# Optimization experiments

Measured on AMD Instinct MI355X. Metric: run time of the kernel, lower is better.

The kernel has to match this reference:

```python
import jax, jax.numpy as jnp
import numpy as np

N_EMBD = 1024
N_HEAD = 16
BLOCK_SIZE = 2048


def setup_inputs() -> dict:
    key = jax.random.key(0)
    k1, k2, k3 = jax.random.split(key, 3)
    B, T, C = 2, 2048, N_EMBD
    x = jax.random.normal(k1, (B, T, C), dtype=jnp.float32)
    # Dense(3*n_embd, use_bias=False): kernel [C, 3C]
    Wqkv = jax.random.normal(k2, (C, 3 * C), dtype=jnp.float32) * (1.0 / np.sqrt(C))
    # Output Dense(n_embd): kernel [C, C] + bias [C]
    Wout = jax.random.normal(k3, (C, C), dtype=jnp.float32) * (1.0 / np.sqrt(C))
    bout = jnp.zeros((C,), dtype=jnp.float32)
    return {"x": x, "Wqkv": Wqkv, "Wout": Wout, "bout": bout}


def reference(x, Wqkv, Wout, bout):
    B, T, C = x.shape
    H = N_HEAD
    hs = C // H  # head_size

    qkv = x @ Wqkv                       # [B, T, 3C]
    q, k, v = jnp.split(qkv, 3, axis=-1)  # each [B, T, C]
    q = q.reshape(B, T, H, hs).transpose(0, 2, 1, 3)  # [B, H, T, hs]
    k = k.reshape(B, T, H, hs).transpose(0, 2, 1, 3)
    v = v.reshape(B, T, H, hs).transpose(0, 2, 1, 3)

    att = jnp.einsum("bhqd,bhkd->bhqk", q, k) * (hs ** -0.5)  # [B, H, T, T]
    T_use = min(T, BLOCK_SIZE)
    mask = jnp.tril(jnp.ones((T_use, T_use), dtype=bool))
    att = jnp.where(mask, att, -jnp.inf)
    att = jax.nn.softmax(att, axis=-1)
    # dropout: deterministic (training=False) -> identity

    out = jnp.einsum("bhqk,bhkd->bhqd", att, v)  # [B, H, T, hs]
    out = out.transpose(0, 2, 1, 3).reshape(B, T, C)
    out = out @ Wout + bout
    return out
```

## Files before the change

### kernel.cpp

```cpp
#include <hip/hip_runtime.h>
#include <cstdint>
#include <cstddef>

#define BB 2
#define TT 2048
#define CC 1024
#define HH 16
#define HS 64
#define MM (BB*TT)
#define N1 (3*CC)

#define PST2 40

#define QSCALE 0.1803368801111243f

typedef __bf16 bf16_t;
typedef bf16_t bf16x8 __attribute__((ext_vector_type(8)));
typedef float  floatx4 __attribute__((ext_vector_type(4)));

__device__ __forceinline__ bf16_t f2bf(float f) {
    uint32_t u = __builtin_bit_cast(uint32_t, f);
    u += 0x7FFFu + ((u >> 16) & 1u);
    unsigned short s = (unsigned short)(u >> 16);
    return __builtin_bit_cast(bf16_t, s);
}

__device__ __forceinline__ void load_lds16(const bf16_t* g, bf16_t* l) {
    __builtin_amdgcn_global_load_lds((__attribute__((address_space(1))) void*)g,
                                     (__attribute__((address_space(3))) void*)l,
                                     16, 0, 0);
}

__global__ __launch_bounds__(256) void k_pack(const float* __restrict__ src,
                                              bf16_t* __restrict__ dst) {
    size_t i = ((size_t)blockIdx.x * 256 + threadIdx.x) * 8;
    float4 a = *(const float4*)(src + i);
    float4 b = *(const float4*)(src + i + 4);
    bf16x8 o;
    o[0] = f2bf(a.x); o[1] = f2bf(a.y); o[2] = f2bf(a.z); o[3] = f2bf(a.w);
    o[4] = f2bf(b.x); o[5] = f2bf(b.y); o[6] = f2bf(b.z); o[7] = f2bf(b.w);
    *(bf16x8*)(dst + i) = o;
}

__global__ __launch_bounds__(256) void k_transpose(const float* __restrict__ src,
                                                   bf16_t* __restrict__ dst,
                                                   int R, int Ccol) {
    __shared__ bf16_t tile[32][33];
    int c0 = blockIdx.x * 32, r0 = blockIdx.y * 32;
    int tx = threadIdx.x, ty = threadIdx.y;
    for (int i = ty; i < 32; i += 8)
        tile[i][tx] = f2bf(src[(size_t)(r0 + i) * Ccol + c0 + tx]);
    __syncthreads();
    for (int i = ty; i < 32; i += 8)
        dst[(size_t)(c0 + i) * R + r0 + tx] = tile[tx][i];
}

__device__ __forceinline__ void gemm_core(const bf16_t* __restrict__ A,
                                          const bf16_t* __restrict__ Bt,
                                          bf16_t* As, bf16_t* Bs,
                                          int m0, int n0, int K,
                                          floatx4 acc[4][4]) {
    const int tid = threadIdx.x;
    const int wave = tid >> 6, lane = tid & 63;
    const int quad = lane >> 4, lrow = lane & 15;
    const int wm = wave >> 1, wn = wave & 1;
    const int lsub = lane >> 2;
    const int kc = lane & 3;

    for (int kk = 0; kk < K; kk += 32) {
        for (int s = 0; s < 2; ++s) {
            int rg = wave * 2 + s;
            const bf16_t* ga = A  + (size_t)(m0 + rg * 16 + lsub) * K + kk + kc * 8;
            const bf16_t* gb = Bt + (size_t)(n0 + rg * 16 + lsub) * K + kk + kc * 8;
            load_lds16(ga, As + rg * 512);
            load_lds16(gb, Bs + rg * 512);
        }
        __syncthreads();
        bf16x8 af[4], bfr[4];
        for (int i = 0; i < 4; ++i)
            af[i] = *(const bf16x8*)(As + (wm * 64 + i * 16 + lrow) * 32 + quad * 8);
        for (int j = 0; j < 4; ++j)
            bfr[j] = *(const bf16x8*)(Bs + (wn * 64 + j * 16 + lrow) * 32 + quad * 8);
        for (int i = 0; i < 4; ++i)
            for (int j = 0; j < 4; ++j)
                acc[i][j] = __builtin_amdgcn_mfma_f32_16x16x32_bf16(af[i], bfr[j], acc[i][j], 0, 0, 0);
        __syncthreads();
    }
}

__global__ __launch_bounds__(256, 2) void k_gemm_qkv(const bf16_t* __restrict__ x,
                                                     const bf16_t* __restrict__ Wt,
                                                     bf16_t* __restrict__ qb,
                                                     bf16_t* __restrict__ kb,
                                                     bf16_t* __restrict__ vn) {
    __shared__ bf16_t As[128 * 32];
    __shared__ bf16_t Bs[128 * 32];
    const int m0 = blockIdx.y * 128, n0 = blockIdx.x * 128;
    floatx4 acc[4][4];
    for (int i = 0; i < 4; ++i)
        for (int j = 0; j < 4; ++j)
            acc[i][j] = floatx4{0.f, 0.f, 0.f, 0.f};
    gemm_core(x, Wt, As, Bs, m0, n0, CC, acc);

    const int tid = threadIdx.x, wave = tid >> 6, lane = tid & 63;
    const int quad = lane >> 4, lrow = lane & 15;
    const int wm = wave >> 1, wn = wave & 1;
    for (int i = 0; i < 4; ++i)
        for (int j = 0; j < 4; ++j) {
            int gn = n0 + wn * 64 + j * 16 + lrow;
            int which = gn >> 10, c = gn & 1023, h = c >> 6, d = c & 63;
            for (int r = 0; r < 4; ++r) {
                int gm = m0 + wm * 64 + i * 16 + quad * 4 + r;
                int b = gm >> 11, t = gm & 2047;
                float val = acc[i][j][r];
                if (which == 0)
                    qb[((size_t)(b * HH + h) * TT + t) * HS + d] = f2bf(val * QSCALE);
                else if (which == 1)
                    kb[((size_t)(b * HH + h) * TT + t) * HS + d] = f2bf(val);
                else
                    vn[((size_t)(b * HH + h) * TT + t) * HS + d] = f2bf(val);
            }
        }
}

__global__ __launch_bounds__(256) void k_vperm(const bf16_t* __restrict__ vn,
                                               bf16_t* __restrict__ vt) {
    __shared__ bf16_t tile[64][72];
    const int tid = threadIdx.x;
    const int bh = blockIdx.x & 31, tb = blockIdx.x >> 5;
    const bf16_t* src = vn + ((size_t)bh * TT + tb * 64) * HS;

    for (int h = 0; h < 2; ++h) {
        int r = (tid >> 3) + h * 32;
        int c8 = (tid & 7) * 8;
        *(bf16x8*)(&tile[r][c8]) = *(const bf16x8*)(src + (size_t)r * HS + c8);
    }
    __syncthreads();

    bf16_t* dst = vt + (size_t)bh * HS * TT + tb * 64;
    const int a   = tid & 15;
    const int blk = ((tid >> 4) & 1) * 32;
    const int dg  = tid >> 5;
    for (int k = 0; k < 8; ++k) {
        int d = dg * 8 + k;
        uint32_t lo = (uint32_t)__builtin_bit_cast(unsigned short, tile[blk + a][d]);
        uint32_t hi = (uint32_t)__builtin_bit_cast(unsigned short, tile[blk + a + 16][d]);
        *(uint32_t*)(dst + (size_t)d * TT + blk + 2 * a) = lo | (hi << 16);
    }
}

__global__ __launch_bounds__(128, 2) void k_attn(const bf16_t* __restrict__ qb,
                                                 const bf16_t* __restrict__ kb,
                                                 const bf16_t* __restrict__ vt,
                                                 bf16_t* __restrict__ y) {
    __shared__ bf16_t Kb[2][32 * 72];
    __shared__ bf16_t Vb[2][64 * 40];
    __shared__ bf16_t Ps[2][32 * PST2];
    const int tid = threadIdx.x;
    const int w = tid >> 6, lane = tid & 63;
    const int quad = lane >> 4, lrow = lane & 15;
    const int bh = blockIdx.x & 31;
    const int g = blockIdx.x >> 5;
    const int t2 = g >> 3, u = g & 7;
    const int qg = (t2 == 0) ? (31 - u) : (t2 == 1) ? u : (t2 == 2) ? (23 - u) : (8 + u);
    const int q0 = qg * 64 + w * 32;
    const int kend = qg * 2 + w + 1;
    const int ntmax = qg * 2 + 2;

    const bf16_t* Qg = qb + (size_t)bh * TT * HS;
    const bf16_t* Kg = kb + (size_t)bh * TT * HS;
    const bf16_t* Vg = vt + (size_t)bh * HS * TT;

    const int skey = tid >> 2, scol = (tid & 3) * 16;
    const int svrow = tid >> 1, svcol = (tid & 1) * 16;

    bf16x8 kra, krb, vra, vrb;
    {
        const bf16_t* gk = Kg + (size_t)skey * HS + scol;
        kra = *(const bf16x8*)(gk);
        krb = *(const bf16x8*)(gk + 8);
        const bf16_t* gv = Vg + (size_t)svrow * TT + svcol;
        vra = *(const bf16x8*)(gv);
        vrb = *(const bf16x8*)(gv + 8);
        *(bf16x8*)(&Kb[0][skey * 72 + scol])     = kra;
        *(bf16x8*)(&Kb[0][skey * 72 + scol + 8]) = krb;
        *(bf16x8*)(&Vb[0][svrow * 40 + svcol])     = vra;
        *(bf16x8*)(&Vb[0][svrow * 40 + svcol + 8]) = vrb;
    }

    bf16x8 aq[2][2];
    for (int tq = 0; tq < 2; ++tq)
        for (int c = 0; c < 2; ++c)
            aq[tq][c] = *(const bf16x8*)(Qg + (size_t)(q0 + tq * 16 + lrow) * HS + c * 32 + quad * 8);

    floatx4 o[2][4];
    for (int tq = 0; tq < 2; ++tq)
        for (int dc = 0; dc < 4; ++dc) o[tq][dc] = floatx4{0.f, 0.f, 0.f, 0.f};
    float lsum[2][4] = {{0.f,0.f,0.f,0.f},{0.f,0.f,0.f,0.f}};

    uint32_t* P32 = (uint32_t*)(&Ps[w][0]);
    const bf16_t* Pr = &Ps[w][0];
    const int wrow0 = quad * 4;

    for (int t = 0; t < ntmax; ++t) {
        __syncthreads();
        if (t + 1 < ntmax) {
            const bf16_t* gk = Kg + (size_t)((t + 1) * 32 + skey) * HS + scol;
            kra = *(const bf16x8*)(gk);
            krb = *(const bf16x8*)(gk + 8);
            const bf16_t* gv = Vg + (size_t)svrow * TT + (t + 1) * 32 + svcol;
            vra = *(const bf16x8*)(gv);
            vrb = *(const bf16x8*)(gv + 8);
        }
        if (t < kend) {
            const bf16_t* Kt = &Kb[t & 1][0];
            const bf16_t* Vt = &Vb[t & 1][0];
            bf16x8 bk0 = *(const bf16x8*)(Kt + lrow * 72 + quad * 8);
            bf16x8 bk1 = *(const bf16x8*)(Kt + lrow * 72 + 32 + quad * 8);
            bf16x8 bk2 = *(const bf16x8*)(Kt + (16 + lrow) * 72 + quad * 8);
            bf16x8 bk3 = *(const bf16x8*)(Kt + (16 + lrow) * 72 + 32 + quad * 8);
            floatx4 s00 = floatx4{0.f,0.f,0.f,0.f}, s01 = s00, s10 = s00, s11 = s00;
            s00 = __builtin_amdgcn_mfma_f32_16x16x32_bf16(aq[0][0], bk0, s00, 0, 0, 0);
            s00 = __builtin_amdgcn_mfma_f32_16x16x32_bf16(aq[0][1], bk1, s00, 0, 0, 0);
            s01 = __builtin_amdgcn_mfma_f32_16x16x32_bf16(aq[0][0], bk2, s01, 0, 0, 0);
            s01 = __builtin_amdgcn_mfma_f32_16x16x32_bf16(aq[0][1], bk3, s01, 0, 0, 0);
            s10 = __builtin_amdgcn_mfma_f32_16x16x32_bf16(aq[1][0], bk0, s10, 0, 0, 0);
            s10 = __builtin_amdgcn_mfma_f32_16x16x32_bf16(aq[1][1], bk1, s10, 0, 0, 0);
            s11 = __builtin_amdgcn_mfma_f32_16x16x32_bf16(aq[1][0], bk2, s11, 0, 0, 0);
            s11 = __builtin_amdgcn_mfma_f32_16x16x32_bf16(aq[1][1], bk3, s11, 0, 0, 0);

            bf16x8 bv0 = *(const bf16x8*)(Vt + (0  + lrow) * 40 + quad * 8);
            bf16x8 bv1 = *(const bf16x8*)(Vt + (16 + lrow) * 40 + quad * 8);
            bf16x8 bv2 = *(const bf16x8*)(Vt + (32 + lrow) * 40 + quad * 8);
            bf16x8 bv3 = *(const bf16x8*)(Vt + (48 + lrow) * 40 + quad * 8);

            if (t < kend - 1) {
                for (int r = 0; r < 4; ++r) {
                    float e00 = __builtin_amdgcn_exp2f(s00[r]);
                    float e01 = __builtin_amdgcn_exp2f(s01[r]);
                    float e10 = __builtin_amdgcn_exp2f(s10[r]);
                    float e11 = __builtin_amdgcn_exp2f(s11[r]);
                    lsum[0][r] += e00 + e01;
                    lsum[1][r] += e10 + e11;
                    uint32_t pk0 = __builtin_amdgcn_perm(
                        __builtin_bit_cast(uint32_t, e01) + 0x8000u,
                        __builtin_bit_cast(uint32_t, e00) + 0x8000u, 0x07060302u);
                    uint32_t pk1 = __builtin_amdgcn_perm(
                        __builtin_bit_cast(uint32_t, e11) + 0x8000u,
                        __builtin_bit_cast(uint32_t, e10) + 0x8000u, 0x07060302u);
                    P32[(wrow0 + r) * 20 + lrow]      = pk0;
                    P32[(wrow0 + r + 16) * 20 + lrow] = pk1;
                }
            } else {
                for (int r = 0; r < 4; ++r) {
                    bool keep = lrow <= quad * 4 + r;
                    float e00 = keep ? __builtin_amdgcn_exp2f(s00[r]) : 0.f;
                    float e01 = 0.f; (void)s01;
                    float e10 = __builtin_amdgcn_exp2f(s10[r]);
                    float e11 = keep ? __builtin_amdgcn_exp2f(s11[r]) : 0.f;
                    lsum[0][r] += e00 + e01;
                    lsum[1][r] += e10 + e11;
                    uint32_t pk0 = __builtin_amdgcn_perm(
                        __builtin_bit_cast(uint32_t, e01) + 0x8000u,
                        __builtin_bit_cast(uint32_t, e00) + 0x8000u, 0x07060302u);
                    uint32_t pk1 = __builtin_amdgcn_perm(
                        __builtin_bit_cast(uint32_t, e11) + 0x8000u,
                        __builtin_bit_cast(uint32_t, e10) + 0x8000u, 0x07060302u);
                    P32[(wrow0 + r) * 20 + lrow]      = pk0;
                    P32[(wrow0 + r + 16) * 20 + lrow] = pk1;
                }
            }
            asm volatile("s_waitcnt lgkmcnt(0)" ::: "memory");

            bf16x8 pa0 = *(const bf16x8*)(Pr + (size_t)lrow * PST2 + quad * 8);
            bf16x8 pa1 = *(const bf16x8*)(Pr + (size_t)(16 + lrow) * PST2 + quad * 8);
            o[0][0] = __builtin_amdgcn_mfma_f32_16x16x32_bf16(pa0, bv0, o[0][0], 0, 0, 0);
            o[0][1] = __builtin_amdgcn_mfma_f32_16x16x32_bf16(pa0, bv1, o[0][1], 0, 0, 0);
            o[0][2] = __builtin_amdgcn_mfma_f32_16x16x32_bf16(pa0, bv2, o[0][2], 0, 0, 0);
            o[0][3] = __builtin_amdgcn_mfma_f32_16x16x32_bf16(pa0, bv3, o[0][3], 0, 0, 0);
            o[1][0] = __builtin_amdgcn_mfma_f32_16x16x32_bf16(pa1, bv0, o[1][0], 0, 0, 0);
            o[1][1] = __builtin_amdgcn_mfma_f32_16x16x32_bf16(pa1, bv1, o[1][1], 0, 0, 0);
            o[1][2] = __builtin_amdgcn_mfma_f32_16x16x32_bf16(pa1, bv2, o[1][2], 0, 0, 0);
            o[1][3] = __builtin_amdgcn_mfma_f32_16x16x32_bf16(pa1, bv3, o[1][3], 0, 0, 0);
        }
        if (t + 1 < ntmax) {
            bf16_t* Kn = &Kb[(t + 1) & 1][0];
            bf16_t* Vn = &Vb[(t + 1) & 1][0];
            *(bf16x8*)(Kn + skey * 72 + scol)     = kra;
            *(bf16x8*)(Kn + skey * 72 + scol + 8) = krb;
            *(bf16x8*)(Vn + svrow * 40 + svcol)     = vra;
            *(bf16x8*)(Vn + svrow * 40 + svcol + 8) = vrb;
        }
    }

    const int b = bh >> 4, h = bh & 15;
    for (int tq = 0; tq < 2; ++tq)
        for (int r = 0; r < 4; ++r) {
            float s = lsum[tq][r];
            s += __shfl_xor(s, 1, 64);
            s += __shfl_xor(s, 2, 64);
            s += __shfl_xor(s, 4, 64);
            s += __shfl_xor(s, 8, 64);
            float inv = 1.0f / s;
            int q = q0 + tq * 16 + quad * 4 + r;
            for (int dc = 0; dc < 4; ++dc)
                y[(size_t)(b * TT + q) * CC + h * HS + dc * 16 + lrow] = f2bf(o[tq][dc][r] * inv);
        }
}

__global__ __launch_bounds__(256, 2) void k_gemm_out(const bf16_t* __restrict__ yin,
                                                     const bf16_t* __restrict__ Wt,
                                                     const float* __restrict__ bias,
                                                     float* __restrict__ out) {
    __shared__ bf16_t As[128 * 32];
    __shared__ bf16_t Bs[128 * 32];
    const int m0 = blockIdx.y * 128, n0 = blockIdx.x * 128;
    floatx4 acc[4][4];
    for (int i = 0; i < 4; ++i)
        for (int j = 0; j < 4; ++j)
            acc[i][j] = floatx4{0.f, 0.f, 0.f, 0.f};
    gemm_core(yin, Wt, As, Bs, m0, n0, CC, acc);

    const int tid = threadIdx.x, wave = tid >> 6, lane = tid & 63;
    const int quad = lane >> 4, lrow = lane & 15;
    const int wm = wave >> 1, wn = wave & 1;
    for (int i = 0; i < 4; ++i)
        for (int j = 0; j < 4; ++j) {
            int gn = n0 + wn * 64 + j * 16 + lrow;
            float bb = bias[gn];
            for (int r = 0; r < 4; ++r) {
                int gm = m0 + wm * 64 + i * 16 + quad * 4 + r;
                out[(size_t)gm * CC + gn] = acc[i][j][r] + bb;
            }
        }
}

extern "C" void kernel_launch(void* const* d_in, const int* in_sizes, int n_in,
                              void* d_out, int out_size, void* d_ws, size_t ws_size,
                              hipStream_t stream) {
    (void)in_sizes; (void)n_in; (void)out_size; (void)ws_size;
    const float* x    = (const float*)d_in[0];
    const float* Wqkv = (const float*)d_in[1];
    const float* Wout = (const float*)d_in[2];
    const float* bout = (const float*)d_in[3];
    float* out = (float*)d_out;

    bf16_t* xb  = (bf16_t*)d_ws;
    bf16_t* Wt1 = xb + (size_t)MM * CC;
    bf16_t* Wt2 = Wt1 + (size_t)N1 * CC;
    bf16_t* qb  = Wt2 + (size_t)CC * CC;
    bf16_t* kb  = qb + (size_t)BB * HH * TT * HS;
    bf16_t* vb  = kb + (size_t)BB * HH * TT * HS;
    bf16_t* yb  = vb + (size_t)BB * HH * TT * HS;
    bf16_t* vn  = yb;

    k_pack<<<dim3((size_t)MM * CC / (256 * 8)), 256, 0, stream>>>(x, xb);
    k_transpose<<<dim3(N1 / 32, CC / 32), dim3(32, 8), 0, stream>>>(Wqkv, Wt1, CC, N1);
    k_transpose<<<dim3(CC / 32, CC / 32), dim3(32, 8), 0, stream>>>(Wout, Wt2, CC, CC);
    k_gemm_qkv<<<dim3(N1 / 128, MM / 128), 256, 0, stream>>>(xb, Wt1, qb, kb, vn);
    k_vperm<<<dim3(32 * 32), 256, 0, stream>>>(vn, vb);
    k_attn<<<dim3(32 * 32), 128, 0, stream>>>(qb, kb, vb, yb);
    k_gemm_out<<<dim3(CC / 128, MM / 128), 256, 0, stream>>>(yb, Wt2, bout, out);
}
```

Measured before the change: 190.2 us.

## Split attention over key chunks with atomic accumulation and separate normalize pass

The attention kernel is now split along the key dimension into chunks of 256 keys, giving 144 blocks per head instead of 32. Partial unnormalized outputs and row sums are accumulated in fp32 with atomicAdd into scratch buffers, and a new k_norm kernel divides and packs the result to bf16. Row sums are computed by an extra MFMA against a vector of ones, and the bf16 rounding bias is dropped so P is truncated. The aim is better load balance and occupancy across the causal triangle, at the cost of two memsets, many atomics, an extra kernel and reuse of the output and weight buffers as scratch.

```diff
diff --git a/kernel.cpp b/kernel.cpp
--- a/kernel.cpp
+++ b/kernel.cpp
@@ -152,7 +152,8 @@
 __global__ __launch_bounds__(128, 2) void k_attn(const bf16_t* __restrict__ qb,
                                                  const bf16_t* __restrict__ kb,
                                                  const bf16_t* __restrict__ vt,
-                                                 bf16_t* __restrict__ y) {
+                                                 float* __restrict__ o_accum,
+                                                 float* __restrict__ l_acc) {
     __shared__ bf16_t Kb[2][32 * 72];
     __shared__ bf16_t Vb[2][64 * 40];
     __shared__ bf16_t Ps[2][32 * PST2];
@@ -160,12 +161,19 @@
     const int w = tid >> 6, lane = tid & 63;
     const int quad = lane >> 4, lrow = lane & 15;
     const int bh = blockIdx.x & 31;
-    const int g = blockIdx.x >> 5;
-    const int t2 = g >> 3, u = g & 7;
-    const int qg = (t2 == 0) ? (31 - u) : (t2 == 1) ? u : (t2 == 2) ? (23 - u) : (8 + u);
+    const int j = blockIdx.x >> 5;
+    int s = 0;
+    #pragma unroll
+    for (int ss = 0; ss < 7; ++ss) if (j >= 2 * (ss + 2) * (ss + 1)) s = ss + 1;
+    const int rem = j - 2 * s * (s + 1);
+    const int qg = 4 * s + rem / (s + 1);
+    const int kc = rem - (rem / (s + 1)) * (s + 1);
+
     const int q0 = qg * 64 + w * 32;
-    const int kend = qg * 2 + w + 1;
-    const int ntmax = qg * 2 + 2;
+    const int key0 = kc * 256;
+    const int ct = min(8, qg * 2 + 2 - kc * 8);
+    const int kendl = qg * 2 + w + 1 - kc * 8;
+    const int kw = min(kendl, ct);
 
     const bf16_t* Qg = qb + (size_t)bh * TT * HS;
     const bf16_t* Kg = kb + (size_t)bh * TT * HS;
@@ -176,10 +184,10 @@
 
     bf16x8 kra, krb, vra, vrb;
     {
-        const bf16_t* gk = Kg + (size_t)skey * HS + scol;
+        const bf16_t* gk = Kg + (size_t)(key0 + skey) * HS + scol;
         kra = *(const bf16x8*)(gk);
         krb = *(const bf16x8*)(gk + 8);
-        const bf16_t* gv = Vg + (size_t)svrow * TT + svcol;
+        const bf16_t* gv = Vg + (size_t)svrow * TT + key0 + svcol;
         vra = *(const bf16x8*)(gv);
         vrb = *(const bf16x8*)(gv + 8);
         *(bf16x8*)(&Kb[0][skey * 72 + scol])     = kra;
@@ -193,26 +201,29 @@
         for (int c = 0; c < 2; ++c)
             aq[tq][c] = *(const bf16x8*)(Qg + (size_t)(q0 + tq * 16 + lrow) * HS + c * 32 + quad * 8);
 
+    const bf16_t onebf = __builtin_bit_cast(bf16_t, (unsigned short)0x3F80);
+    bf16x8 bones = {onebf, onebf, onebf, onebf, onebf, onebf, onebf, onebf};
+
     floatx4 o[2][4];
     for (int tq = 0; tq < 2; ++tq)
         for (int dc = 0; dc < 4; ++dc) o[tq][dc] = floatx4{0.f, 0.f, 0.f, 0.f};
-    float lsum[2][4] = {{0.f,0.f,0.f,0.f},{0.f,0.f,0.f,0.f}};
+    floatx4 ol[2] = {floatx4{0.f,0.f,0.f,0.f}, floatx4{0.f,0.f,0.f,0.f}};
 
     uint32_t* P32 = (uint32_t*)(&Ps[w][0]);
     const bf16_t* Pr = &Ps[w][0];
     const int wrow0 = quad * 4;
 
-    for (int t = 0; t < ntmax; ++t) {
+    for (int t = 0; t < ct; ++t) {
         __syncthreads();
-        if (t + 1 < ntmax) {
-            const bf16_t* gk = Kg + (size_t)((t + 1) * 32 + skey) * HS + scol;
+        if (t + 1 < ct) {
+            const bf16_t* gk = Kg + (size_t)(key0 + (t + 1) * 32 + skey) * HS + scol;
             kra = *(const bf16x8*)(gk);
             krb = *(const bf16x8*)(gk + 8);
-            const bf16_t* gv = Vg + (size_t)svrow * TT + (t + 1) * 32 + svcol;
+            const bf16_t* gv = Vg + (size_t)svrow * TT + key0 + (t + 1) * 32 + svcol;
             vra = *(const bf16x8*)(gv);
             vrb = *(const bf16x8*)(gv + 8);
         }
-        if (t < kend) {
+        if (t < kw) {
             const bf16_t* Kt = &Kb[t & 1][0];
             const bf16_t* Vt = &Vb[t & 1][0];
             bf16x8 bk0 = *(const bf16x8*)(Kt + lrow * 72 + quad * 8);
@@ -234,20 +245,18 @@
             bf16x8 bv2 = *(const bf16x8*)(Vt + (32 + lrow) * 40 + quad * 8);
             bf16x8 bv3 = *(const bf16x8*)(Vt + (48 + lrow) * 40 + quad * 8);
 
-            if (t < kend - 1) {
+            if (t < kendl - 1) {
                 for (int r = 0; r < 4; ++r) {
                     float e00 = __builtin_amdgcn_exp2f(s00[r]);
                     float e01 = __builtin_amdgcn_exp2f(s01[r]);
                     float e10 = __builtin_amdgcn_exp2f(s10[r]);
                     float e11 = __builtin_amdgcn_exp2f(s11[r]);
-                    lsum[0][r] += e00 + e01;
-                    lsum[1][r] += e10 + e11;
                     uint32_t pk0 = __builtin_amdgcn_perm(
-                        __builtin_bit_cast(uint32_t, e01) + 0x8000u,
-                        __builtin_bit_cast(uint32_t, e00) + 0x8000u, 0x07060302u);
+                        __builtin_bit_cast(uint32_t, e01),
+                        __builtin_bit_cast(uint32_t, e00), 0x07060302u);
                     uint32_t pk1 = __builtin_amdgcn_perm(
-                        __builtin_bit_cast(uint32_t, e11) + 0x8000u,
-                        __builtin_bit_cast(uint32_t, e10) + 0x8000u, 0x07060302u);
+                        __builtin_bit_cast(uint32_t, e11),
+                        __builtin_bit_cast(uint32_t, e10), 0x07060302u);
                     P32[(wrow0 + r) * 20 + lrow]      = pk0;
                     P32[(wrow0 + r + 16) * 20 + lrow] = pk1;
                 }
@@ -258,14 +267,12 @@
                     float e01 = 0.f; (void)s01;
                     float e10 = __builtin_amdgcn_exp2f(s10[r]);
                     float e11 = keep ? __builtin_amdgcn_exp2f(s11[r]) : 0.f;
-                    lsum[0][r] += e00 + e01;
-                    lsum[1][r] += e10 + e11;
                     uint32_t pk0 = __builtin_amdgcn_perm(
-                        __builtin_bit_cast(uint32_t, e01) + 0x8000u,
-                        __builtin_bit_cast(uint32_t, e00) + 0x8000u, 0x07060302u);
+                        __builtin_bit_cast(uint32_t, e01),
+                        __builtin_bit_cast(uint32_t, e00), 0x07060302u);
                     uint32_t pk1 = __builtin_amdgcn_perm(
-                        __builtin_bit_cast(uint32_t, e11) + 0x8000u,
-                        __builtin_bit_cast(uint32_t, e10) + 0x8000u, 0x07060302u);
+                        __builtin_bit_cast(uint32_t, e11),
+                        __builtin_bit_cast(uint32_t, e10), 0x07060302u);
                     P32[(wrow0 + r) * 20 + lrow]      = pk0;
                     P32[(wrow0 + r + 16) * 20 + lrow] = pk1;
                 }
@@ -278,12 +285,14 @@
             o[0][1] = __builtin_amdgcn_mfma_f32_16x16x32_bf16(pa0, bv1, o[0][1], 0, 0, 0);
             o[0][2] = __builtin_amdgcn_mfma_f32_16x16x32_bf16(pa0, bv2, o[0][2], 0, 0, 0);
             o[0][3] = __builtin_amdgcn_mfma_f32_16x16x32_bf16(pa0, bv3, o[0][3], 0, 0, 0);
+            ol[0]   = __builtin_amdgcn_mfma_f32_16x16x32_bf16(pa0, bones, ol[0], 0, 0, 0);
             o[1][0] = __builtin_amdgcn_mfma_f32_16x16x32_bf16(pa1, bv0, o[1][0], 0, 0, 0);
             o[1][1] = __builtin_amdgcn_mfma_f32_16x16x32_bf16(pa1, bv1, o[1][1], 0, 0, 0);
             o[1][2] = __builtin_amdgcn_mfma_f32_16x16x32_bf16(pa1, bv2, o[1][2], 0, 0, 0);
             o[1][3] = __builtin_amdgcn_mfma_f32_16x16x32_bf16(pa1, bv3, o[1][3], 0, 0, 0);
-        }
-        if (t + 1 < ntmax) {
+            ol[1]   = __builtin_amdgcn_mfma_f32_16x16x32_bf16(pa1, bones, ol[1], 0, 0, 0);
+        }
+        if (t + 1 < ct) {
             bf16_t* Kn = &Kb[(t + 1) & 1][0];
             bf16_t* Vn = &Vb[(t + 1) & 1][0];
             *(bf16x8*)(Kn + skey * 72 + scol)     = kra;
@@ -293,19 +302,35 @@
         }
     }
 
-    const int b = bh >> 4, h = bh & 15;
     for (int tq = 0; tq < 2; ++tq)
         for (int r = 0; r < 4; ++r) {
-            float s = lsum[tq][r];
-            s += __shfl_xor(s, 1, 64);
-            s += __shfl_xor(s, 2, 64);
-            s += __shfl_xor(s, 4, 64);
-            s += __shfl_xor(s, 8, 64);
-            float inv = 1.0f / s;
             int q = q0 + tq * 16 + quad * 4 + r;
+            float* dst = o_accum + ((size_t)bh * TT + q) * HS + lrow;
             for (int dc = 0; dc < 4; ++dc)
-                y[(size_t)(b * TT + q) * CC + h * HS + dc * 16 + lrow] = f2bf(o[tq][dc][r] * inv);
-        }
+                atomicAdd(dst + dc * 16, o[tq][dc][r]);
+            if (lrow == 0)
+                atomicAdd(l_acc + (size_t)bh * TT + q, ol[tq][r]);
+        }
+}
+
+__global__ __launch_bounds__(256) void k_norm(const float* __restrict__ o_accum,
+                                              const float* __restrict__ l_acc,
+                                              bf16_t* __restrict__ yb) {
+    int idx = blockIdx.x * 256 + threadIdx.x;
+    int d8 = idx & 7;
+    int q  = (idx >> 3) & (TT - 1);
+    int bh = idx >> 14;
+    float inv = 1.0f / l_acc[(size_t)bh * TT + q];
+    const float* src = o_accum + ((size_t)bh * TT + q) * HS + d8 * 8;
+    float4 a = *(const float4*)(src);
+    float4 b = *(const float4*)(src + 4);
+    bf16x8 r;
+    r[0] = f2bf(a.x * inv); r[1] = f2bf(a.y * inv);
+    r[2] = f2bf(a.z * inv); r[3] = f2bf(a.w * inv);
+    r[4] = f2bf(b.x * inv); r[5] = f2bf(b.y * inv);
+    r[6] = f2bf(b.z * inv); r[7] = f2bf(b.w * inv);
+    int bb = bh >> 4, h = bh & 15;
+    *(bf16x8*)(yb + ((size_t)(bb * TT + q)) * CC + h * HS + d8 * 8) = r;
 }
 
 __global__ __launch_bounds__(256, 2) void k_gemm_out(const bf16_t* __restrict__ yin,
@@ -353,12 +378,17 @@
     bf16_t* vb  = kb + (size_t)BB * HH * TT * HS;
     bf16_t* yb  = vb + (size_t)BB * HH * TT * HS;
     bf16_t* vn  = yb;
+    float*  o_accum = (float*)d_out;
+    float*  l_acc   = (float*)Wt1;
 
     k_pack<<<dim3((size_t)MM * CC / (256 * 8)), 256, 0, stream>>>(x, xb);
     k_transpose<<<dim3(N1 / 32, CC / 32), dim3(32, 8), 0, stream>>>(Wqkv, Wt1, CC, N1);
     k_transpose<<<dim3(CC / 32, CC / 32), dim3(32, 8), 0, stream>>>(Wout, Wt2, CC, CC);
     k_gemm_qkv<<<dim3(N1 / 128, MM / 128), 256, 0, stream>>>(xb, Wt1, qb, kb, vn);
+    hipMemsetAsync(o_accum, 0, (size_t)MM * CC * sizeof(float), stream);
+    hipMemsetAsync(l_acc, 0, (size_t)BB * HH * TT * sizeof(float), stream);
     k_vperm<<<dim3(32 * 32), 256, 0, stream>>>(vn, vb);
-    k_attn<<<dim3(32 * 32), 128, 0, stream>>>(qb, kb, vb, yb);
+    k_attn<<<dim3(144 * 32), 128, 0, stream>>>(qb, kb, vb, o_accum, l_acc);
+    k_norm<<<dim3(BB * HH * TT * 8 / 256), 256, 0, stream>>>(o_accum, l_acc, yb);
     k_gemm_out<<<dim3(CC / 128, MM / 128), 256, 0, stream>>>(yb, Wt2, bout, out);
 }
```

Measured after the change: 235.4 us. +23.8%, slower.
